# Optimization experiments

Hardware: AMD Instinct MI355X
Metric: run time of the kernel (lower is better)

The kernel has to match this reference:

```python
import jax, jax.numpy as jnp
import numpy as np
import math

D_MODEL = 512
NHEAD = 8
HEAD_DIM = D_MODEL // NHEAD
MAX_REL = 128
B, T, S = 4, 2048, 2048


def setup_inputs() -> dict:
    key = jax.random.key(0)
    ks = jax.random.split(key, 16)
    sc = 1.0 / math.sqrt(D_MODEL)
    inp = {
        "query": jax.random.normal(ks[0], (B, T, D_MODEL), jnp.float32),
        "key": jax.random.normal(ks[1], (B, S, D_MODEL), jnp.float32),
        "value": jax.random.normal(ks[2], (B, S, D_MODEL), jnp.float32),
        "Wq": jax.random.normal(ks[3], (D_MODEL, D_MODEL), jnp.float32) * sc,
        "bq": jnp.zeros((D_MODEL,), jnp.float32),
        "Wk": jax.random.normal(ks[4], (D_MODEL, D_MODEL), jnp.float32) * sc,
        "bk": jnp.zeros((D_MODEL,), jnp.float32),
        "Wv": jax.random.normal(ks[5], (D_MODEL, D_MODEL), jnp.float32) * sc,
        "bv": jnp.zeros((D_MODEL,), jnp.float32),
        "Wo": jax.random.normal(ks[6], (D_MODEL, D_MODEL), jnp.float32) * sc,
        "bo": jnp.zeros((D_MODEL,), jnp.float32),
        "rel_emb": jax.random.normal(ks[7], (2 * MAX_REL + 1, NHEAD), jnp.float32) * 0.02,
    }
    return inp


def reference(query, key, value, Wq, bq, Wk, bk, Wv, bv, Wo, bo, rel_emb):
    # linear projections (torch Linear: x @ W.T + b), split heads -> [B,H,T,Dh]
    def proj(x, W, b, L):
        return (x @ W.T + b).reshape(B, L, NHEAD, HEAD_DIM).transpose(0, 2, 1, 3)

    q = proj(query, Wq, bq, T)
    k = proj(key, Wk, bk, S)
    v = proj(value, Wv, bv, S)

    scores = jnp.einsum("bhtd,bhsd->bhts", q, k) / math.sqrt(HEAD_DIM)

    # relative position bias lookup: rel[t,s] = clamp(t-s) + max_rel -> [H,T,S]
    rel = jnp.arange(T)[:, None] - jnp.arange(S)[None, :]
    rel = jnp.clip(rel, -MAX_REL, MAX_REL) + MAX_REL
    bias = rel_emb[rel].transpose(2, 0, 1)  # [H,T,S]
    scores = scores + bias[None]

    w = jax.nn.softmax(scores, axis=-1)  # dropout p used in eval mode -> identity
    out = jnp.einsum("bhts,bhsd->bhtd", w, v)
    out = out.transpose(0, 2, 1, 3).reshape(B, T, D_MODEL)
    return out @ Wo.T + bo
```

## Files before the change

### kernel.cpp

```cpp
#include <hip/hip_runtime.h>

typedef __attribute__((ext_vector_type(4))) float f32x4;
typedef __attribute__((ext_vector_type(16))) float f32x16;
typedef __attribute__((ext_vector_type(4))) unsigned short u16x4;
typedef __attribute__((ext_vector_type(8))) unsigned short u16x8;
typedef __attribute__((ext_vector_type(4))) unsigned int u32x4;
typedef __attribute__((ext_vector_type(8))) __bf16 bf16x8;

#define SZX_E ((size_t)4 * 2048 * 512)
#define SZW_E ((size_t)512 * 512)

__device__ __forceinline__ unsigned short f2bf(float f) {
  unsigned int u = __builtin_bit_cast(unsigned int, f);
  u += 0x7fffu + ((u >> 16) & 1u);
  return (unsigned short)(u >> 16);
}

__device__ __forceinline__ bf16x8 ld_bf8(const unsigned short* p) {
  return __builtin_bit_cast(bf16x8, *(const u16x8*)p);
}

__device__ __forceinline__ f32x4 mfma16(bf16x8 a, bf16x8 b, f32x4 c) {
  return __builtin_amdgcn_mfma_f32_16x16x32_bf16(a, b, c, 0, 0, 0);
}

__device__ __forceinline__ f32x16 mfma32(bf16x8 a, bf16x8 b, f32x16 c) {
  return __builtin_amdgcn_mfma_f32_32x32x16_bf16(a, b, c, 0, 0, 0);
}

__device__ __forceinline__ unsigned int cvt_pk_bf16(float lo, float hi) {
  unsigned int r;
  asm("v_cvt_pk_bf16_f32 %0, %1, %2" : "=v"(r) : "v"(lo), "v"(hi));
  return r;
}

__device__ __forceinline__ void plane32_swap(unsigned int& a, unsigned int& b) {
  asm("v_permlane32_swap_b32 %0, %1" : "+v"(a), "+v"(b));
}

__device__ __forceinline__ float exp2_fast(float x) {
  float r;
  asm("v_exp_f32 %0, %1" : "=v"(r) : "v"(x));
  return r;
}

__device__ __forceinline__ void gload16(const void* g, void* l) {
  __builtin_amdgcn_global_load_lds(
      (const __attribute__((address_space(1))) unsigned int*)g,
      (__attribute__((address_space(3))) unsigned int*)l, 16, 0, 0);
}

__global__ __launch_bounds__(256) void cvt_all(const float* __restrict__ q_,
                                               const float* __restrict__ k_,
                                               const float* __restrict__ v_,
                                               const float* __restrict__ wq_,
                                               const float* __restrict__ wk_,
                                               const float* __restrict__ wv_,
                                               const float* __restrict__ wo_,
                                               unsigned short* __restrict__ out) {
  const int bq = blockIdx.x;
  const float* src;
  size_t segbase, li;
  if (bq < 12288) {
    const int s = bq >> 12;
    src = (s == 0) ? q_ : (s == 1) ? k_ : v_;
    li = (size_t)(bq & 4095) * 256 + threadIdx.x;
    segbase = (size_t)s * 4194304;
  } else {
    const int s = (bq - 12288) >> 8;
    src = (s == 0) ? wq_ : (s == 1) ? wk_ : (s == 2) ? wv_ : wo_;
    li = (size_t)((bq - 12288) & 255) * 256 + threadIdx.x;
    segbase = 12582912 + (size_t)s * 262144;
  }
  const f32x4 v = *(const f32x4*)(src + li * 4);
  u16x4 r;
  r[0] = f2bf(v[0]); r[1] = f2bf(v[1]); r[2] = f2bf(v[2]); r[3] = f2bf(v[3]);
  *(u16x4*)(out + segbase + li * 4) = r;
}

__global__ __launch_bounds__(256) void gemm_qkv(const unsigned short* __restrict__ base,
                                                const float* __restrict__ bq,
                                                const float* __restrict__ bk,
                                                const float* __restrict__ bv,
                                                unsigned short* __restrict__ outb) {
  __shared__ unsigned short Asb[2][4096];
  __shared__ unsigned short Bsb[2][4096];
  const int z = blockIdx.z;
  const unsigned short* A = base + (size_t)z * SZX_E;
  const unsigned short* Bw = base + 3 * SZX_E + (size_t)z * SZW_E;
  const float* bias = (z == 0) ? bq : (z == 1) ? bk : bv;

  const int tid = threadIdx.x;
  const int l = tid & 63;
  const int w = tid >> 6;
  const int g = l >> 4;
  const int lr = l & 15;
  const int bid = blockIdx.x + (blockIdx.y << 2);
  const int lgg = (bid & 7) * 32 + (bid >> 3);
  const int nB = (lgg & 3) * 128;
  const int mB = (lgg >> 2) * 128;
  const int m0 = (w >> 1) * 64;
  const int n0 = (w & 1) * 64;
  const int ubase = tid & ~63;

  auto stage = [&](int bufi, int kk) {
#pragma unroll
    for (int i = 0; i < 2; i++) {
      const int idx = i * 256 + tid;
      const int ub = i * 256 + ubase;
      const int r = idx >> 2, c = idx & 3;
      gload16((const char*)A + ((size_t)(mB + r) * 512 + kk + c * 8) * 2,
              (char*)&Asb[bufi][0] + ub * 16);
      gload16((const char*)Bw + ((size_t)(nB + r) * 512 + kk + c * 8) * 2,
              (char*)&Bsb[bufi][0] + ub * 16);
    }
  };

  f32x4 acc[4][4];
#pragma unroll
  for (int i = 0; i < 4; i++)
#pragma unroll
    for (int j = 0; j < 4; j++) acc[i][j] = f32x4{0.f, 0.f, 0.f, 0.f};

  stage(0, 0);
  __syncthreads();
  int buf = 0;

  for (int ks = 0; ks < 16; ++ks) {
    if (ks < 15) stage(buf ^ 1, (ks + 1) * 32);
    bf16x8 af[4], bfr[4];
#pragma unroll
    for (int t = 0; t < 4; t++) {
      af[t] = ld_bf8(&Asb[buf][(m0 + t * 16 + lr) * 32 + g * 8]);
      bfr[t] = ld_bf8(&Bsb[buf][(n0 + t * 16 + lr) * 32 + g * 8]);
    }
#pragma unroll
    for (int i = 0; i < 4; i++)
#pragma unroll
      for (int j = 0; j < 4; j++)
        acc[i][j] = mfma16(af[i], bfr[j], acc[i][j]);
    __syncthreads();
    buf ^= 1;
  }

  unsigned short* outz = outb + (size_t)z * SZX_E;
#pragma unroll
  for (int j = 0; j < 4; j++) {
    const int n = nB + n0 + j * 16 + lr;
    const float bn = bias[n];
#pragma unroll
    for (int i = 0; i < 4; i++) {
#pragma unroll
      for (int r = 0; r < 4; r++) {
        const int m = mB + m0 + i * 16 + g * 4 + r;
        const float v = acc[i][j][r] + bn;
        if (z < 2) {
          outz[(size_t)m * 512 + n] = f2bf(v);
        } else {
          const int bb = m >> 11, s = m & 2047;
          const int hh = n >> 6, d = n & 63;
          outz[((size_t)((bb * 8 + hh) * 64 + d) << 11) + s] = f2bf(v);
        }
      }
    }
  }
}

__global__ __launch_bounds__(256) void gemm_o(const unsigned short* __restrict__ A,
                                              const unsigned short* __restrict__ Bw,
                                              const float* __restrict__ bias,
                                              float* __restrict__ Cout) {
  __shared__ unsigned short Asb[2][4096];
  __shared__ unsigned short Bsb[2][4096];
  const int tid = threadIdx.x;
  const int l = tid & 63;
  const int w = tid >> 6;
  const int g = l >> 4;
  const int lr = l & 15;
  const int bid = blockIdx.x + (blockIdx.y << 2);
  const int lgg = (bid & 7) * 32 + (bid >> 3);
  const int nB = (lgg & 3) * 128;
  const int mB = (lgg >> 2) * 128;
  const int m0 = (w >> 1) * 64;
  const int n0 = (w & 1) * 64;
  const int ubase = tid & ~63;

  auto stage = [&](int bufi, int kk) {
#pragma unroll
    for (int i = 0; i < 2; i++) {
      const int idx = i * 256 + tid;
      const int ub = i * 256 + ubase;
      const int r = idx >> 2, c = idx & 3;
      gload16((const char*)A + ((size_t)(mB + r) * 512 + kk + c * 8) * 2,
              (char*)&Asb[bufi][0] + ub * 16);
      gload16((const char*)Bw + ((size_t)(nB + r) * 512 + kk + c * 8) * 2,
              (char*)&Bsb[bufi][0] + ub * 16);
    }
  };

  f32x4 acc[4][4];
#pragma unroll
  for (int i = 0; i < 4; i++)
#pragma unroll
    for (int j = 0; j < 4; j++) acc[i][j] = f32x4{0.f, 0.f, 0.f, 0.f};

  stage(0, 0);
  __syncthreads();
  int buf = 0;

  for (int ks = 0; ks < 16; ++ks) {
    if (ks < 15) stage(buf ^ 1, (ks + 1) * 32);
    bf16x8 af[4], bfr[4];
#pragma unroll
    for (int t = 0; t < 4; t++) {
      af[t] = ld_bf8(&Asb[buf][(m0 + t * 16 + lr) * 32 + g * 8]);
      bfr[t] = ld_bf8(&Bsb[buf][(n0 + t * 16 + lr) * 32 + g * 8]);
    }
#pragma unroll
    for (int i = 0; i < 4; i++)
#pragma unroll
      for (int j = 0; j < 4; j++)
        acc[i][j] = mfma16(af[i], bfr[j], acc[i][j]);
    __syncthreads();
    buf ^= 1;
  }

#pragma unroll
  for (int j = 0; j < 4; j++) {
    const int n = nB + n0 + j * 16 + lr;
    const float bn = bias[n];
#pragma unroll
    for (int i = 0; i < 4; i++) {
#pragma unroll
      for (int r = 0; r < 4; r++) {
        const int m = mB + m0 + i * 16 + g * 4 + r;
        Cout[(size_t)m * 512 + n] = acc[i][j][r] + bn;
      }
    }
  }
}

__global__ __launch_bounds__(256, 2) void attn_kernel(const unsigned short* __restrict__ Qp,
                                                      const unsigned short* __restrict__ Kp,
                                                      const unsigned short* __restrict__ Vt,
                                                      const float* __restrict__ rel_emb,
                                                      unsigned short* __restrict__ At) {
  __shared__ float bias_s[257];
  __shared__ unsigned short K_lds[2][4096];
  __shared__ unsigned short V_lds[2][4096];
  const int bid0 = blockIdx.x;
  const int lg = (bid0 & 7) * 64 + (bid0 >> 3);
  const int qb = lg & 15;
  const int h = (lg >> 4) & 7;
  const int b = lg >> 7;
  const int tid = threadIdx.x;
  const int lane = tid & 63, w = tid >> 6;
  const int hi = lane >> 5, q31 = lane & 31;
  const int q0w = qb * 128 + w * 32;
  const int tq = q0w + q31;
  const float SCL = 0.125f * 1.44269504f;

  const bool isK = (w < 2);
  const char* sbase = isK ? (const char*)Kp + ((size_t)b * 2048 * 512 + h * 64) * 2
                          : (const char*)Vt + ((size_t)(b * 8 + h) * 64 * 2048) * 2;
  const size_t step = isK ? (size_t)64 * 1024 : 128;
  const int i0 = (w & 1) * 4;
  const int rr0 = (i0 + 0) * 8 + (lane >> 3), ch0 = (lane & 7) ^ (rr0 & 7);
  const int rr1 = (i0 + 1) * 8 + (lane >> 3), ch1 = (lane & 7) ^ (rr1 & 7);
  const int rr2 = (i0 + 2) * 8 + (lane >> 3), ch2 = (lane & 7) ^ (rr2 & 7);
  const int rr3 = (i0 + 3) * 8 + (lane >> 3), ch3 = (lane & 7) ^ (rr3 & 7);
  const size_t rstr = isK ? 1024 : 4096;
  const char* gp0 = sbase + (size_t)rr0 * rstr + ch0 * 16;
  const char* gp1 = sbase + (size_t)rr1 * rstr + ch1 * 16;
  const char* gp2 = sbase + (size_t)rr2 * rstr + ch2 * 16;
  const char* gp3 = sbase + (size_t)rr3 * rstr + ch3 * 16;
  char* db0 = (isK ? (char*)&K_lds[0][0] : (char*)&V_lds[0][0]) + i0 * 1024;
  char* db1 = (isK ? (char*)&K_lds[1][0] : (char*)&V_lds[1][0]) + i0 * 1024;

  auto STAGE = [&](char* dbase) {
    gload16(gp0, dbase);
    gload16(gp1, dbase + 1024);
    gload16(gp2, dbase + 2048);
    gload16(gp3, dbase + 3072);
    gp0 += step; gp1 += step; gp2 += step; gp3 += step;
  };

  for (int i = tid; i < 257; i += 256) bias_s[i] = rel_emb[i * 8 + h] * 1.44269504f;
  STAGE(db0);
  __syncthreads();
  const float bias_lo = bias_s[0], bias_hi = bias_s[256];

  const unsigned short* qptr = Qp + (size_t)(b * 2048 + tq) * 512 + h * 64 + hi * 8;
  const bf16x8 qf0 = ld_bf8(qptr);
  const bf16x8 qf1 = ld_bf8(qptr + 16);
  const bf16x8 qf2 = ld_bf8(qptr + 32);
  const bf16x8 qf3 = ld_bf8(qptr + 48);

  const int rswz = q31 & 7;
  int koff[4], voff[4];
#pragma unroll
  for (int c = 0; c < 4; c++) koff[c] = q31 * 64 + (((2 * c + hi) ^ rswz) << 3);
#pragma unroll
  for (int ks = 0; ks < 4; ks++) voff[ks] = q31 * 64 + (((ks * 2 + hi) ^ rswz) << 3);

  const f32x16 z16 = {0.f, 0.f, 0.f, 0.f, 0.f, 0.f, 0.f, 0.f,
                      0.f, 0.f, 0.f, 0.f, 0.f, 0.f, 0.f, 0.f};
  f32x16 o_lo = z16, o_hi = z16;
  float l_run = 0.f;

  auto TILE = [&](const unsigned short* kb, const unsigned short* vb, int s0) {
    bf16x8 kfl0 = ld_bf8(kb + koff[0]);
    bf16x8 kfh0 = ld_bf8(kb + 2048 + koff[0]);
    bf16x8 kfl1 = ld_bf8(kb + koff[1]);
    bf16x8 kfh1 = ld_bf8(kb + 2048 + koff[1]);
    bf16x8 kfl2 = ld_bf8(kb + koff[2]);
    bf16x8 kfh2 = ld_bf8(kb + 2048 + koff[2]);
    bf16x8 kfl3 = ld_bf8(kb + koff[3]);
    bf16x8 kfh3 = ld_bf8(kb + 2048 + koff[3]);
    bf16x8 vl[4], vh[4];
#pragma unroll
    for (int ks = 0; ks < 4; ks++) {
      vl[ks] = ld_bf8(vb + voff[ks]);
      vh[ks] = ld_bf8(vb + 2048 + voff[ks]);
    }

    f32x16 sa, sb;
    sa = mfma32(kfl0, qf0, z16);
    sb = mfma32(kfh0, qf0, z16);
    sa = mfma32(kfl1, qf1, sa);
    sb = mfma32(kfh1, qf1, sb);
    sa = mfma32(kfl2, qf2, sa);
    sb = mfma32(kfh2, qf2, sb);
    sa = mfma32(kfl3, qf3, sa);
    sb = mfma32(kfh3, qf3, sb);

    const int relmin = q0w - s0 - 63;
    const int relmax = q0w + 31 - s0;
    float SCL2, off0;
    if (relmin >= 128 || relmax <= -128) {
      SCL2 = SCL;
      off0 = (relmin >= 128) ? bias_hi : bias_lo;
    } else {
#pragma unroll
      for (int r = 0; r < 16; r++) {
        const int rowA = (r & 3) + 8 * (r >> 2) + 4 * hi;
        const int rA = tq - s0 - rowA;
        const int rB = rA - 32;
        const int iA = (rA < -128 ? -128 : (rA > 128 ? 128 : rA)) + 128;
        const int iB = (rB < -128 ? -128 : (rB > 128 ? 128 : rB)) + 128;
        sa[r] = fmaf(sa[r], SCL, bias_s[iA]);
        sb[r] = fmaf(sb[r], SCL, bias_s[iB]);
      }
      SCL2 = 1.f;
      off0 = 0.f;
    }

#pragma unroll
    for (int r = 0; r < 16; r++) {
      sa[r] = exp2_fast(fmaf(sa[r], SCL2, off0));
      sb[r] = exp2_fast(fmaf(sb[r], SCL2, off0));
    }
    float s8[8];
#pragma unroll
    for (int i = 0; i < 8; i++)
      s8[i] = (sa[i] + sa[i + 8]) + (sb[i] + sb[i + 8]);
    float ps = ((s8[0] + s8[1]) + (s8[2] + s8[3])) + ((s8[4] + s8[5]) + (s8[6] + s8[7]));
    ps += __shfl_xor(ps, 32, 64);
    l_run += ps;

    bf16x8 pa[4];
#pragma unroll
    for (int ks = 0; ks < 4; ks++) {
      const int c8 = (ks & 1) * 8;
      const f32x16& src = (ks < 2) ? sa : sb;
      unsigned int a0 = cvt_pk_bf16(src[c8 + 0], src[c8 + 1]);
      unsigned int b0 = cvt_pk_bf16(src[c8 + 4], src[c8 + 5]);
      unsigned int a1 = cvt_pk_bf16(src[c8 + 2], src[c8 + 3]);
      unsigned int b1 = cvt_pk_bf16(src[c8 + 6], src[c8 + 7]);
      plane32_swap(a0, b0);
      plane32_swap(a1, b1);
      pa[ks] = __builtin_bit_cast(bf16x8, u32x4{a0, a1, b0, b1});
    }

#pragma unroll
    for (int ks = 0; ks < 4; ks++) {
      o_lo = mfma32(pa[ks], vl[ks], o_lo);
      o_hi = mfma32(pa[ks], vh[ks], o_hi);
    }
  };

  const unsigned short* K0 = &K_lds[0][0];
  const unsigned short* K1 = &K_lds[1][0];
  const unsigned short* V0 = &V_lds[0][0];
  const unsigned short* V1 = &V_lds[1][0];

  for (int t = 0; t < 32; t += 2) {
    STAGE(db1);
    TILE(K0, V0, t * 64);
    __syncthreads();
    if (t + 2 < 32) STAGE(db0);
    TILE(K1, V1, (t + 1) * 64);
    __syncthreads();
  }

  const float inv = 1.f / l_run;
#pragma unroll
  for (int r2 = 0; r2 < 16; r2++) {
    const int ro = (r2 & 3) + 8 * (r2 >> 2) + 4 * hi;
    const float rr = __shfl(inv, ro, 64);
    unsigned short* op = At + (size_t)(b * 2048 + q0w + ro) * 512 + h * 64;
    op[q31] = f2bf(o_lo[r2] * rr);
    op[32 + q31] = f2bf(o_hi[r2] * rr);
  }
}

extern "C" void kernel_launch(void* const* d_in, const int* in_sizes, int n_in,
                              void* d_out, int out_size, void* d_ws, size_t ws_size,
                              hipStream_t stream) {
  const float* query = (const float*)d_in[0];
  const float* key   = (const float*)d_in[1];
  const float* value = (const float*)d_in[2];
  const float* Wq = (const float*)d_in[3];
  const float* bq = (const float*)d_in[4];
  const float* Wk = (const float*)d_in[5];
  const float* bk = (const float*)d_in[6];
  const float* Wv = (const float*)d_in[7];
  const float* bv = (const float*)d_in[8];
  const float* Wo = (const float*)d_in[9];
  const float* bo = (const float*)d_in[10];
  const float* rel = (const float*)d_in[11];

  char* ws = (char*)d_ws;
  unsigned short* base = (unsigned short*)ws;
  unsigned short* wo = base + 3 * SZX_E + 3 * SZW_E;
  unsigned short* Qp = base + 3 * SZX_E + 4 * SZW_E;
  unsigned short* Kp = Qp + SZX_E;
  unsigned short* Vt = Kp + SZX_E;
  unsigned short* At = Vt + SZX_E;

  cvt_all<<<dim3(13312), dim3(256), 0, stream>>>(query, key, value, Wq, Wk, Wv, Wo, base);

  dim3 blk(256);
  gemm_qkv<<<dim3(4, 64, 3), blk, 0, stream>>>(base, bq, bk, bv, Qp);

  attn_kernel<<<dim3(512), blk, 0, stream>>>(Qp, Kp, Vt, rel, At);

  gemm_o<<<dim3(4, 64), blk, 0, stream>>>(At, wo, bo, (float*)d_out);
}
```

Before: 102.2 us.

## Triple-buffer K/V LDS staging with partial vmcnt waits in attention loop

Grows the attention kernel's K/V shared-memory staging from two buffers to three and keeps two tile loads in flight. Each step waits only until the oldest tile's loads have landed (vmcnt(4)) plus a barrier, instead of draining all loads with __syncthreads. The aim is to hide global-to-LDS load latency behind the MFMA work. The cost is 16KB more LDS per block, which may reduce occupancy at two blocks per CU, and a more intricate wait-count scheme that relies on how many loads are outstanding.

```diff
diff --git a/kernel.cpp b/kernel.cpp
--- a/kernel.cpp
+++ b/kernel.cpp
@@ -49,6 +49,19 @@
       (const __attribute__((address_space(1))) unsigned int*)g,
       (__attribute__((address_space(3))) unsigned int*)l, 16, 0, 0);
 }
+
+#define VBAR4 do { \
+    asm volatile("s_waitcnt vmcnt(4)" ::: "memory"); \
+    __builtin_amdgcn_sched_barrier(0); \
+    __builtin_amdgcn_s_barrier(); \
+    __builtin_amdgcn_sched_barrier(0); \
+  } while (0)
+#define VBAR0 do { \
+    asm volatile("s_waitcnt vmcnt(0)" ::: "memory"); \
+    __builtin_amdgcn_sched_barrier(0); \
+    __builtin_amdgcn_s_barrier(); \
+    __builtin_amdgcn_sched_barrier(0); \
+  } while (0)
 
 __global__ __launch_bounds__(256) void cvt_all(const float* __restrict__ q_,
                                                const float* __restrict__ k_,
@@ -246,8 +259,8 @@
                                                       const float* __restrict__ rel_emb,
                                                       unsigned short* __restrict__ At) {
   __shared__ float bias_s[257];
-  __shared__ unsigned short K_lds[2][4096];
-  __shared__ unsigned short V_lds[2][4096];
+  __shared__ unsigned short K_lds[3][4096];
+  __shared__ unsigned short V_lds[3][4096];
   const int bid0 = blockIdx.x;
   const int lg = (bid0 & 7) * 64 + (bid0 >> 3);
   const int qb = lg & 15;
@@ -274,8 +287,9 @@
   const char* gp1 = sbase + (size_t)rr1 * rstr + ch1 * 16;
   const char* gp2 = sbase + (size_t)rr2 * rstr + ch2 * 16;
   const char* gp3 = sbase + (size_t)rr3 * rstr + ch3 * 16;
-  char* db0 = (isK ? (char*)&K_lds[0][0] : (char*)&V_lds[0][0]) + i0 * 1024;
-  char* db1 = (isK ? (char*)&K_lds[1][0] : (char*)&V_lds[1][0]) + i0 * 1024;
+  char* dbA = (isK ? (char*)&K_lds[0][0] : (char*)&V_lds[0][0]) + i0 * 1024;
+  char* dbB = (isK ? (char*)&K_lds[1][0] : (char*)&V_lds[1][0]) + i0 * 1024;
+  char* dbC = (isK ? (char*)&K_lds[2][0] : (char*)&V_lds[2][0]) + i0 * 1024;
 
   auto STAGE = [&](char* dbase) {
     gload16(gp0, dbase);
@@ -285,16 +299,17 @@
     gp0 += step; gp1 += step; gp2 += step; gp3 += step;
   };
 
-  for (int i = tid; i < 257; i += 256) bias_s[i] = rel_emb[i * 8 + h] * 1.44269504f;
-  STAGE(db0);
-  __syncthreads();
-  const float bias_lo = bias_s[0], bias_hi = bias_s[256];
-
   const unsigned short* qptr = Qp + (size_t)(b * 2048 + tq) * 512 + h * 64 + hi * 8;
   const bf16x8 qf0 = ld_bf8(qptr);
   const bf16x8 qf1 = ld_bf8(qptr + 16);
   const bf16x8 qf2 = ld_bf8(qptr + 32);
   const bf16x8 qf3 = ld_bf8(qptr + 48);
+
+  STAGE(dbA);
+  STAGE(dbB);
+  for (int i = tid; i < 257; i += 256) bias_s[i] = rel_emb[i * 8 + h] * 1.44269504f;
+  __syncthreads();
+  const float bias_lo = bias_s[0], bias_hi = bias_s[256];
 
   const int rswz = q31 & 7;
   int koff[4], voff[4];
@@ -391,17 +406,19 @@
 
   const unsigned short* K0 = &K_lds[0][0];
   const unsigned short* K1 = &K_lds[1][0];
+  const unsigned short* K2 = &K_lds[2][0];
   const unsigned short* V0 = &V_lds[0][0];
   const unsigned short* V1 = &V_lds[1][0];
-
-  for (int t = 0; t < 32; t += 2) {
-    STAGE(db1);
-    TILE(K0, V0, t * 64);
-    __syncthreads();
-    if (t + 2 < 32) STAGE(db0);
-    TILE(K1, V1, (t + 1) * 64);
-    __syncthreads();
-  }
+  const unsigned short* V2 = &V_lds[2][0];
+
+  for (int it = 0; it < 10; ++it) {
+    const int u = it * 3;
+    VBAR4; STAGE(dbC); TILE(K0, V0, u * 64);
+    VBAR4; STAGE(dbA); TILE(K1, V1, (u + 1) * 64);
+    VBAR4; STAGE(dbB); TILE(K2, V2, (u + 2) * 64);
+  }
+  VBAR4; TILE(K0, V0, 30 * 64);
+  VBAR0; TILE(K1, V1, 31 * 64);
 
   const float inv = 1.f / l_run;
 #pragma unroll
```

After: 102.0 us (median of 2 runs). Within noise of the previous version (-0.2%).
